# Performance work log

Measured on AMD Instinct MI355X. Metric: run time of the kernel, lower is better.

The kernel has to match this reference:

```python
import jax, jax.numpy as jnp
import numpy as np

NUM_HEADS = 8
OUT_DIM = 32


def setup_inputs() -> dict:
    key = jax.random.key(0)
    ks = jax.random.split(key, 9)
    N, E, IN = 50000, 800000, 256
    HD = NUM_HEADS * OUT_DIM
    s = 1.0 / np.sqrt(IN)
    return {
        "h": jax.random.normal(ks[0], (N, IN), jnp.float32),
        "Wq": jax.random.normal(ks[1], (HD, IN), jnp.float32) * s,
        "bq": jax.random.normal(ks[2], (HD,), jnp.float32) * 0.01,
        "Wk": jax.random.normal(ks[3], (HD, IN), jnp.float32) * s,
        "bk": jax.random.normal(ks[4], (HD,), jnp.float32) * 0.01,
        "Wv": jax.random.normal(ks[5], (HD, IN), jnp.float32) * s,
        "bv": jax.random.normal(ks[6], (HD,), jnp.float32) * 0.01,
        "src": jax.random.randint(ks[7], (E,), 0, N, jnp.int32),
        "dst": jax.random.randint(ks[8], (E,), 0, N, jnp.int32),
    }


def reference(h, Wq, bq, Wk, bk, Wv, bv, src, dst):
    N = h.shape[0]
    H, D = NUM_HEADS, OUT_DIM
    # node projections -> [N, H, D]
    Q = (h @ Wq.T + bq).reshape(N, H, D)
    K = (h @ Wk.T + bk).reshape(N, H, D)
    V = (h @ Wv.T + bv).reshape(N, H, D)
    scale = jnp.asarray(np.sqrt(D), h.dtype)
    # per-edge scores: dot(K[src], Q[dst]) over D -> [E, H]
    score = jnp.exp(jnp.clip((K[src] * Q[dst]).sum(-1) / scale, -5.0, 5.0))
    # segment-softmax denominator over destination nodes -> [N, H]
    z = jax.ops.segment_sum(score, dst, num_segments=N)
    alpha = score / z[dst]  # [E, H]; every edge's dst has z > 0
    # weighted aggregation: sum over in-edges of alpha * V[src] -> [N, H, D]
    wV = jax.ops.segment_sum(V[src] * alpha[:, :, None], dst, num_segments=N)
    return wV
```

## Files before the change

### kernel.cpp

```cpp
#include <hip/hip_runtime.h>
#include <hip/hip_bf16.h>


typedef __attribute__((ext_vector_type(8))) short short8;
typedef __attribute__((ext_vector_type(8))) unsigned short ushortx8;
typedef __attribute__((ext_vector_type(4))) unsigned short ushortx4;
typedef __attribute__((ext_vector_type(4))) float floatx4;
typedef __attribute__((ext_vector_type(4))) int intx4;

__device__ __forceinline__ void g2l16(const void* g, void* l) {
    __builtin_amdgcn_global_load_lds(
        (const __attribute__((address_space(1))) unsigned int*)g,
        (__attribute__((address_space(3))) unsigned int*)l, 16, 0, 0);
}

__device__ __forceinline__ float bf2f(unsigned short u) {
    union { unsigned int i; float f; } c; c.i = ((unsigned int)u) << 16; return c.f;
}
__device__ __forceinline__ unsigned short f2bf(float f) {
    __hip_bfloat16 b = __float2bfloat16(f);
    return *reinterpret_cast<unsigned short*>(&b);
}

__global__ __launch_bounds__(256) void cvt_bf16(const float* __restrict__ src,
                                                unsigned short* __restrict__ dst, int n4) {
    int i = blockIdx.x * 256 + threadIdx.x;
    if (i >= n4) return;
    floatx4 f = __builtin_nontemporal_load((const floatx4*)src + i);
    ushortx4 u;
    u.x = f2bf(f.x); u.y = f2bf(f.y); u.z = f2bf(f.z); u.w = f2bf(f.w);
    ((ushortx4*)dst)[i] = u;
}

__global__ __launch_bounds__(256) void cvt_w3(const float* __restrict__ Wq,
                                              const float* __restrict__ Wk,
                                              const float* __restrict__ Wv,
                                              unsigned short* __restrict__ Wb, int n4) {
    int mat = blockIdx.y;
    const float* src = (mat == 0) ? Wq : (mat == 1) ? Wk : Wv;
    int i = blockIdx.x * 256 + threadIdx.x;
    if (i >= n4) return;
    floatx4 f = __builtin_nontemporal_load((const floatx4*)src + i);
    ushortx4 u;
    u.x = f2bf(f.x); u.y = f2bf(f.y); u.z = f2bf(f.z); u.w = f2bf(f.w);
    ((ushortx4*)(Wb + (size_t)mat * 65536))[i] = u;
}

__global__ __launch_bounds__(256) void qkv_gemm_mfma(
    const unsigned short* __restrict__ hb, const unsigned short* __restrict__ Wb,
    const float* __restrict__ bq, const float* __restrict__ bk, const float* __restrict__ bv,
    unsigned short* __restrict__ Qb, unsigned short* __restrict__ KV, int N)
{
    __shared__ unsigned short Ast[2][128 * 32];
    __shared__ unsigned short Bst[2][128 * 32];

    const int tid = threadIdx.x;
    const int wave = tid >> 6;
    const int lane = tid & 63;
    const int m = lane & 15;
    const int q = lane >> 4;
    const int wr = wave >> 1, wc = wave & 1;

    const int mbase = blockIdx.x * 128;
    const int mat = blockIdx.y >> 1;
    const int colbase = (blockIdx.y & 1) * 128;
    const int wrow0 = blockIdx.y * 128;

    const float* bias = (mat == 0) ? bq : (mat == 1) ? bk : bv;

    floatx4 acc[4][4] = {};

    for (int kk = 0; kk < 256; kk += 64) {
#pragma unroll
        for (int c = 0; c < 2; c++) {
#pragma unroll
            for (int t = 0; t < 2; t++) {
                int f = t * 256 + tid;
                int row = f >> 2, kc = f & 3;
                int grow = mbase + row; if (grow > N - 1) grow = N - 1;
                g2l16(hb + (size_t)grow * 256 + kk + c * 32 + kc * 8,
                      Ast[c] + (size_t)(t * 256 + wave * 64) * 8);
            }
#pragma unroll
            for (int t = 0; t < 2; t++) {
                int f = t * 256 + tid;
                int row = f >> 2, kc = f & 3;
                g2l16(Wb + (size_t)(wrow0 + row) * 256 + kk + c * 32 + kc * 8,
                      Bst[c] + (size_t)(t * 256 + wave * 64) * 8);
            }
        }
        __syncthreads();

#pragma unroll
        for (int c = 0; c < 2; c++) {
            short8 a[4], b[4];
#pragma unroll
            for (int i = 0; i < 4; i++) {
                int r = wr * 64 + i * 16 + m;
                a[i] = *(const short8*)&Ast[c][r * 32 + q * 8];
            }
#pragma unroll
            for (int j = 0; j < 4; j++) {
                int cc = wc * 64 + j * 16 + m;
                b[j] = *(const short8*)&Bst[c][cc * 32 + q * 8];
            }
#pragma unroll
            for (int i = 0; i < 4; i++)
#pragma unroll
                for (int j = 0; j < 4; j++)
                    acc[i][j] = __builtin_amdgcn_mfma_f32_16x16x32_bf16(a[i], b[j], acc[i][j], 0, 0, 0);
        }
        __syncthreads();
    }

    float bvj[4];
#pragma unroll
    for (int j = 0; j < 4; j++) bvj[j] = bias[colbase + wc * 64 + j * 16 + m];

    const int col0 = colbase + wc * 64 + m;
#pragma unroll
    for (int i = 0; i < 4; i++) {
#pragma unroll
        for (int r = 0; r < 4; r++) {
            int grow = mbase + wr * 64 + i * 16 + q * 4 + r;
            if (grow < N) {
                if (mat == 0) {
                    unsigned short* op = Qb + (size_t)grow * 256 + col0;
#pragma unroll
                    for (int j = 0; j < 4; j++)
                        __builtin_nontemporal_store(f2bf(acc[i][j][r] + bvj[j]), op + j * 16);
                } else {
                    unsigned short* op = KV + (size_t)grow * 512 + ((mat == 2) ? 256 : 0) + col0;
#pragma unroll
                    for (int j = 0; j < 4; j++)
                        op[j * 16] = f2bf(acc[i][j][r] + bvj[j]);
                }
            }
        }
    }
}

__global__ void count_deg(const int* __restrict__ dst, int* __restrict__ deg, int E) {
    int e4 = (blockIdx.x * 256 + threadIdx.x) * 4;
    if (e4 + 3 < E) {
        intx4 d = __builtin_nontemporal_load((const intx4*)(dst + e4));
        atomicAdd(&deg[d.x], 1); atomicAdd(&deg[d.y], 1);
        atomicAdd(&deg[d.z], 1); atomicAdd(&deg[d.w], 1);
    } else {
        for (int e = e4; e < E; e++) atomicAdd(&deg[dst[e]], 1);
    }
}

#define SCAN_CHUNK 2048

__global__ void scan_phase1(const int* __restrict__ deg, int* __restrict__ partials, int N) {
    __shared__ int sdata[256];
    int base = blockIdx.x * SCAN_CHUNK;
    int sum = 0;
#pragma unroll
    for (int i = 0; i < 8; i++) {
        int idx = base + threadIdx.x + i * 256;
        if (idx < N) sum += deg[idx];
    }
    sdata[threadIdx.x] = sum;
    __syncthreads();
    for (int s = 128; s > 0; s >>= 1) {
        if (threadIdx.x < (unsigned)s) sdata[threadIdx.x] += sdata[threadIdx.x + s];
        __syncthreads();
    }
    if (threadIdx.x == 0) partials[blockIdx.x] = sdata[0];
}

__global__ void scan_phase2(int* __restrict__ partials, int nb) {
    if (threadIdx.x == 0 && blockIdx.x == 0) {
        int run = 0;
        for (int i = 0; i < nb; i++) { int v = partials[i]; partials[i] = run; run += v; }
    }
}

__global__ void scan_phase3(const int* __restrict__ deg, const int* __restrict__ partials,
                            int* __restrict__ offsets, int* __restrict__ cursor, int N, int E) {
    __shared__ int sdata[256];
    int base = blockIdx.x * SCAN_CHUNK;
    int vals[8];
    int sum = 0;
#pragma unroll
    for (int i = 0; i < 8; i++) {
        int idx = base + threadIdx.x * 8 + i;
        vals[i] = (idx < N) ? deg[idx] : 0;
        sum += vals[i];
    }
    sdata[threadIdx.x] = sum;
    __syncthreads();
    for (int s = 1; s < 256; s <<= 1) {
        int v = sdata[threadIdx.x];
        int add = (threadIdx.x >= (unsigned)s) ? sdata[threadIdx.x - s] : 0;
        __syncthreads();
        sdata[threadIdx.x] = v + add;
        __syncthreads();
    }
    int excl = (threadIdx.x == 0) ? 0 : sdata[threadIdx.x - 1];
    int run = partials[blockIdx.x] + excl;
#pragma unroll
    for (int i = 0; i < 8; i++) {
        int idx = base + threadIdx.x * 8 + i;
        if (idx < N) { offsets[idx] = run; cursor[idx] = run; }
        run += vals[i];
    }
    if (blockIdx.x == 0 && threadIdx.x == 0) offsets[N] = E;
}

__global__ void scatter_edges(const int* __restrict__ dst, const int* __restrict__ src,
                              int* __restrict__ cursor, unsigned short* __restrict__ ssorted,
                              int E) {
    int e4 = (blockIdx.x * 256 + threadIdx.x) * 4;
    if (e4 + 3 < E) {
        intx4 d = __builtin_nontemporal_load((const intx4*)(dst + e4));
        intx4 s = __builtin_nontemporal_load((const intx4*)(src + e4));
        ssorted[atomicAdd(&cursor[d.x], 1)] = (unsigned short)s.x;
        ssorted[atomicAdd(&cursor[d.y], 1)] = (unsigned short)s.y;
        ssorted[atomicAdd(&cursor[d.z], 1)] = (unsigned short)s.z;
        ssorted[atomicAdd(&cursor[d.w], 1)] = (unsigned short)s.w;
    } else {
        for (int e = e4; e < E; e++)
            ssorted[atomicAdd(&cursor[dst[e]], 1)] = (unsigned short)src[e];
    }
}

__global__ __launch_bounds__(256) void edge_agg(
    const unsigned short* __restrict__ Qb, const unsigned short* __restrict__ KV,
    const int* __restrict__ offsets, const unsigned short* __restrict__ ssorted,
    float* __restrict__ out, int N)
{
    const int wave = threadIdx.x >> 6;
    const int lane = threadIdx.x & 63;
    const int half = lane >> 5;
    const int hl = lane & 31;
    const int n = blockIdx.x * 4 + wave;
    if (n >= N) return;

    float q[8];
    {
        ushortx8 qu = __builtin_nontemporal_load((const ushortx8*)(Qb + (size_t)n * 256 + hl * 8));
#pragma unroll
        for (int j = 0; j < 8; j++) q[j] = bf2f(qu[j]);
    }

    float acc[8] = {};
    float z = 0.f;
    const int beg = offsets[n], end = offsets[n + 1];
    const int len = end - beg;
    const int mid = beg + ((len + 1) >> 1);
    const float scale = 0.17677669529663687f;

    int i = half ? mid : beg;
    const int i1 = half ? end : mid;

    for (; i + 1 < i1; i += 2) {
        int s0 = __builtin_nontemporal_load(ssorted + i);
        int s1 = __builtin_nontemporal_load(ssorted + i + 1);
        const unsigned short* p0 = KV + (size_t)s0 * 512 + hl * 8;
        const unsigned short* p1 = KV + (size_t)s1 * 512 + hl * 8;
        ushortx8 k0 = *(const ushortx8*)p0;        ushortx8 v0 = *(const ushortx8*)(p0 + 256);
        ushortx8 k1 = *(const ushortx8*)p1;        ushortx8 v1 = *(const ushortx8*)(p1 + 256);

        float d0 = 0.f, d1 = 0.f;
#pragma unroll
        for (int j = 0; j < 8; j++) {
            d0 = fmaf(bf2f(k0[j]), q[j], d0);
            d1 = fmaf(bf2f(k1[j]), q[j], d1);
        }
        d0 += __shfl_xor(d0, 1); d0 += __shfl_xor(d0, 2);
        d1 += __shfl_xor(d1, 1); d1 += __shfl_xor(d1, 2);
        float e0 = __expf(fminf(5.f, fmaxf(-5.f, d0 * scale)));
        float e1 = __expf(fminf(5.f, fmaxf(-5.f, d1 * scale)));
        z += e0 + e1;
#pragma unroll
        for (int j = 0; j < 8; j++) {
            acc[j] = fmaf(e0, bf2f(v0[j]), acc[j]);
            acc[j] = fmaf(e1, bf2f(v1[j]), acc[j]);
        }
    }
    for (; i < i1; i++) {
        int s = __builtin_nontemporal_load(ssorted + i);
        const unsigned short* p = KV + (size_t)s * 512 + hl * 8;
        ushortx8 k8 = *(const ushortx8*)p;
        ushortx8 v8 = *(const ushortx8*)(p + 256);
        float d = 0.f;
#pragma unroll
        for (int j = 0; j < 8; j++) d = fmaf(bf2f(k8[j]), q[j], d);
        d += __shfl_xor(d, 1); d += __shfl_xor(d, 2);
        float sc = __expf(fminf(5.f, fmaxf(-5.f, d * scale)));
        z += sc;
#pragma unroll
        for (int j = 0; j < 8; j++) acc[j] = fmaf(sc, bf2f(v8[j]), acc[j]);
    }

    z += __shfl_xor(z, 32);
#pragma unroll
    for (int j = 0; j < 8; j++) acc[j] += __shfl_xor(acc[j], 32);

    if (half == 0) {
        float inv = (z > 0.f) ? 1.f / z : 0.f;
        floatx4 o0, o1;
        o0[0] = acc[0] * inv; o0[1] = acc[1] * inv; o0[2] = acc[2] * inv; o0[3] = acc[3] * inv;
        o1[0] = acc[4] * inv; o1[1] = acc[5] * inv; o1[2] = acc[6] * inv; o1[3] = acc[7] * inv;
        floatx4* op = (floatx4*)(out + (size_t)n * 256 + hl * 8);
        __builtin_nontemporal_store(o0, op);
        __builtin_nontemporal_store(o1, op + 1);
    }
}

extern "C" void kernel_launch(void* const* d_in, const int* in_sizes, int n_in,
                              void* d_out, int out_size, void* d_ws, size_t ws_size,
                              hipStream_t stream) {
    const float* h  = (const float*)d_in[0];
    const float* Wq = (const float*)d_in[1];
    const float* bq = (const float*)d_in[2];
    const float* Wk = (const float*)d_in[3];
    const float* bk = (const float*)d_in[4];
    const float* Wv = (const float*)d_in[5];
    const float* bv = (const float*)d_in[6];
    const int*   src = (const int*)d_in[7];
    const int*   dst = (const int*)d_in[8];
    float* out = (float*)d_out;

    const int N = in_sizes[0] / 256;
    const int E = in_sizes[7];

    size_t off = 0;
    auto alloc = [&](size_t bytes) {
        void* p = (char*)d_ws + off;
        off += (bytes + 255) & ~(size_t)255;
        return p;
    };
    unsigned short* Qb = (unsigned short*)alloc((size_t)N * 256 * 2);
    unsigned short* KV = (unsigned short*)alloc((size_t)N * 512 * 2);
    unsigned short* hb = (unsigned short*)alloc((size_t)N * 256 * 2);
    unsigned short* Wb = (unsigned short*)alloc((size_t)768 * 256 * 2);
    int* deg      = (int*)alloc((size_t)N * 4);
    int* offsets  = (int*)alloc((size_t)(N + 1) * 4);
    int* cursor   = (int*)alloc((size_t)N * 4);
    int* partials = (int*)alloc(1024 * 4);
    unsigned short* ssorted = (unsigned short*)alloc((size_t)E * 2);

    int n4h = (N * 256) / 4;
    cvt_bf16<<<(n4h + 255) / 256, 256, 0, stream>>>(h, hb, n4h);
    int n4w = (256 * 256) / 4;
    dim3 wgrid((n4w + 255) / 256, 3);
    cvt_w3<<<wgrid, 256, 0, stream>>>(Wq, Wk, Wv, Wb, n4w);

    dim3 ggrid((N + 127) / 128, 6);
    qkv_gemm_mfma<<<ggrid, 256, 0, stream>>>(hb, Wb, bq, bk, bv, Qb, KV, N);

    hipMemsetAsync(deg, 0, (size_t)N * 4, stream);
    int eblocks4 = (E + 1023) / 1024;
    count_deg<<<eblocks4, 256, 0, stream>>>(dst, deg, E);

    int nscan = (N + SCAN_CHUNK - 1) / SCAN_CHUNK;
    scan_phase1<<<nscan, 256, 0, stream>>>(deg, partials, N);
    scan_phase2<<<1, 64, 0, stream>>>(partials, nscan);
    scan_phase3<<<nscan, 256, 0, stream>>>(deg, partials, offsets, cursor, N, E);

    scatter_edges<<<eblocks4, 256, 0, stream>>>(dst, src, cursor, ssorted, E);

    int ablocks = (N + 3) / 4;
    edge_agg<<<ablocks, 256, 0, stream>>>(Qb, KV, offsets, ssorted, out, N);
}
```

Measured before the change: 366.7 us.

## Fuse h/W bf16 conversion and degree counting into one prep kernel, XCD-remap GEMM

Merges the h conversion, weight conversion and degree-count kernels into a single grid-stride prep kernel with role-partitioned blocks. This saves launches and lets the atomic degree counting overlap with the bandwidth-bound conversion. The QKV GEMM moves to a 1D grid with an XCD-aware block remapping, so consecutive tiles that share h rows land on the same XCD for L2 reuse. The cost is fewer, longer-running blocks and more complex index math.

```diff
diff --git a/kernel.cpp b/kernel.cpp
--- a/kernel.cpp
+++ b/kernel.cpp
@@ -22,28 +22,88 @@
     return *reinterpret_cast<unsigned short*>(&b);
 }
 
-__global__ __launch_bounds__(256) void cvt_bf16(const float* __restrict__ src,
-                                                unsigned short* __restrict__ dst, int n4) {
-    int i = blockIdx.x * 256 + threadIdx.x;
-    if (i >= n4) return;
-    floatx4 f = __builtin_nontemporal_load((const floatx4*)src + i);
+__device__ __forceinline__ ushortx4 cvt4(floatx4 f) {
     ushortx4 u;
     u.x = f2bf(f.x); u.y = f2bf(f.y); u.z = f2bf(f.z); u.w = f2bf(f.w);
-    ((ushortx4*)dst)[i] = u;
-}
-
-__global__ __launch_bounds__(256) void cvt_w3(const float* __restrict__ Wq,
-                                              const float* __restrict__ Wk,
-                                              const float* __restrict__ Wv,
-                                              unsigned short* __restrict__ Wb, int n4) {
-    int mat = blockIdx.y;
-    const float* src = (mat == 0) ? Wq : (mat == 1) ? Wk : Wv;
-    int i = blockIdx.x * 256 + threadIdx.x;
-    if (i >= n4) return;
-    floatx4 f = __builtin_nontemporal_load((const floatx4*)src + i);
-    ushortx4 u;
-    u.x = f2bf(f.x); u.y = f2bf(f.y); u.z = f2bf(f.z); u.w = f2bf(f.w);
-    ((ushortx4*)(Wb + (size_t)mat * 65536))[i] = u;
+    return u;
+}
+
+#define PREP_BH 1563
+#define PREP_BW 16
+#define PREP_BD 256
+
+__global__ __launch_bounds__(256) void prep(
+    const float* __restrict__ h, unsigned short* __restrict__ hb,
+    const float* __restrict__ Wq, const float* __restrict__ Wk, const float* __restrict__ Wv,
+    unsigned short* __restrict__ Wb,
+    const int* __restrict__ dst, int* __restrict__ deg,
+    int n4h, int n4w, int E)
+{
+    const int bid = blockIdx.x;
+    const int tid = threadIdx.x;
+    if (bid < PREP_BH) {
+        const int stride = PREP_BH * 256;
+        const floatx4* hs = (const floatx4*)h;
+        ushortx4* hd = (ushortx4*)hb;
+        int i = bid * 256 + tid;
+        for (; i + 3 * stride < n4h; i += 4 * stride) {
+            floatx4 f0 = __builtin_nontemporal_load(hs + i);
+            floatx4 f1 = __builtin_nontemporal_load(hs + i + stride);
+            floatx4 f2 = __builtin_nontemporal_load(hs + i + 2 * stride);
+            floatx4 f3 = __builtin_nontemporal_load(hs + i + 3 * stride);
+            hd[i] = cvt4(f0);
+            hd[i + stride] = cvt4(f1);
+            hd[i + 2 * stride] = cvt4(f2);
+            hd[i + 3 * stride] = cvt4(f3);
+        }
+        for (; i < n4h; i += stride) {
+            floatx4 f = __builtin_nontemporal_load(hs + i);
+            hd[i] = cvt4(f);
+        }
+    } else if (bid < PREP_BH + 3 * PREP_BW) {
+        int b2 = bid - PREP_BH;
+        int mat = b2 / PREP_BW;
+        const floatx4* ws = (const floatx4*)((mat == 0) ? Wq : (mat == 1) ? Wk : Wv);
+        ushortx4* wd = (ushortx4*)(Wb + (size_t)mat * 65536);
+        const int stride = PREP_BW * 256;
+        int i = (b2 % PREP_BW) * 256 + tid;
+        for (; i + 3 * stride < n4w; i += 4 * stride) {
+            floatx4 f0 = __builtin_nontemporal_load(ws + i);
+            floatx4 f1 = __builtin_nontemporal_load(ws + i + stride);
+            floatx4 f2 = __builtin_nontemporal_load(ws + i + 2 * stride);
+            floatx4 f3 = __builtin_nontemporal_load(ws + i + 3 * stride);
+            wd[i] = cvt4(f0);
+            wd[i + stride] = cvt4(f1);
+            wd[i + 2 * stride] = cvt4(f2);
+            wd[i + 3 * stride] = cvt4(f3);
+        }
+        for (; i < n4w; i += stride) {
+            floatx4 f = __builtin_nontemporal_load(ws + i);
+            wd[i] = cvt4(f);
+        }
+    } else {
+        int b3 = bid - PREP_BH - 3 * PREP_BW;
+        const int stride = PREP_BD * 256;
+        const int ne4 = E >> 2;
+        const intx4* ds = (const intx4*)dst;
+        int i = b3 * 256 + tid;
+        for (; i + stride < ne4; i += 2 * stride) {
+            intx4 d0 = __builtin_nontemporal_load(ds + i);
+            intx4 d1 = __builtin_nontemporal_load(ds + i + stride);
+            atomicAdd(&deg[d0.x], 1); atomicAdd(&deg[d0.y], 1);
+            atomicAdd(&deg[d0.z], 1); atomicAdd(&deg[d0.w], 1);
+            atomicAdd(&deg[d1.x], 1); atomicAdd(&deg[d1.y], 1);
+            atomicAdd(&deg[d1.z], 1); atomicAdd(&deg[d1.w], 1);
+        }
+        for (; i < ne4; i += stride) {
+            intx4 d = __builtin_nontemporal_load(ds + i);
+            atomicAdd(&deg[d.x], 1); atomicAdd(&deg[d.y], 1);
+            atomicAdd(&deg[d.z], 1); atomicAdd(&deg[d.w], 1);
+        }
+        if (b3 == 0 && tid == 0) {
+            for (int e = ne4 * 4; e < E; e++) atomicAdd(&deg[dst[e]], 1);
+        }
+    }
 }
 
 __global__ __launch_bounds__(256) void qkv_gemm_mfma(
@@ -61,10 +121,19 @@
     const int q = lane >> 4;
     const int wr = wave >> 1, wc = wave & 1;
 
-    const int mbase = blockIdx.x * 128;
-    const int mat = blockIdx.y >> 1;
-    const int colbase = (blockIdx.y & 1) * 128;
-    const int wrow0 = blockIdx.y * 128;
+    const int nwg = gridDim.x;
+    const int orig = blockIdx.x;
+    const int q8 = nwg >> 3, r8 = nwg & 7;
+    const int xcd = orig & 7;
+    const int wgid = (xcd < r8 ? xcd * (q8 + 1) : r8 * (q8 + 1) + (xcd - r8) * q8)
+                     + (orig >> 3);
+    const int bx = wgid / 6;
+    const int by = wgid % 6;
+
+    const int mbase = bx * 128;
+    const int mat = by >> 1;
+    const int colbase = (by & 1) * 128;
+    const int wrow0 = by * 128;
 
     const float* bias = (mat == 0) ? bq : (mat == 1) ? bk : bv;
 
@@ -137,17 +206,6 @@
                 }
             }
         }
-    }
-}
-
-__global__ void count_deg(const int* __restrict__ dst, int* __restrict__ deg, int E) {
-    int e4 = (blockIdx.x * 256 + threadIdx.x) * 4;
-    if (e4 + 3 < E) {
-        intx4 d = __builtin_nontemporal_load((const intx4*)(dst + e4));
-        atomicAdd(&deg[d.x], 1); atomicAdd(&deg[d.y], 1);
-        atomicAdd(&deg[d.z], 1); atomicAdd(&deg[d.w], 1);
-    } else {
-        for (int e = e4; e < E; e++) atomicAdd(&deg[dst[e]], 1);
     }
 }
 
@@ -344,25 +402,21 @@
     int* partials = (int*)alloc(1024 * 4);
     unsigned short* ssorted = (unsigned short*)alloc((size_t)E * 2);
 
+    hipMemsetAsync(deg, 0, (size_t)N * 4, stream);
     int n4h = (N * 256) / 4;
-    cvt_bf16<<<(n4h + 255) / 256, 256, 0, stream>>>(h, hb, n4h);
     int n4w = (256 * 256) / 4;
-    dim3 wgrid((n4w + 255) / 256, 3);
-    cvt_w3<<<wgrid, 256, 0, stream>>>(Wq, Wk, Wv, Wb, n4w);
-
-    dim3 ggrid((N + 127) / 128, 6);
-    qkv_gemm_mfma<<<ggrid, 256, 0, stream>>>(hb, Wb, bq, bk, bv, Qb, KV, N);
-
-    hipMemsetAsync(deg, 0, (size_t)N * 4, stream);
-    int eblocks4 = (E + 1023) / 1024;
-    count_deg<<<eblocks4, 256, 0, stream>>>(dst, deg, E);
+    prep<<<PREP_BH + 3 * PREP_BW + PREP_BD, 256, 0, stream>>>(
+        h, hb, Wq, Wk, Wv, Wb, dst, deg, n4h, n4w, E);
+
+    int nb6 = ((N + 127) / 128) * 6;
+    qkv_gemm_mfma<<<nb6, 256, 0, stream>>>(hb, Wb, bq, bk, bv, Qb, KV, N);
 
     int nscan = (N + SCAN_CHUNK - 1) / SCAN_CHUNK;
     scan_phase1<<<nscan, 256, 0, stream>>>(deg, partials, N);
     scan_phase2<<<1, 64, 0, stream>>>(partials, nscan);
     scan_phase3<<<nscan, 256, 0, stream>>>(deg, partials, offsets, cursor, N, E);
-
-    scatter_edges<<<eblocks4, 256, 0, stream>>>(dst, src, cursor, ssorted, E);
+    int bc = (E + 1023) / 1024;
+    scatter_edges<<<bc, 256, 0, stream>>>(dst, src, cursor, ssorted, E);
 
     int ablocks = (N + 3) / 4;
     edge_agg<<<ablocks, 256, 0, stream>>>(Qb, KV, offsets, ssorted, out, N);
```

Result: faster. 351.6 us (-4.1%).

## Fuse preprocessing, GEMM and CSR build into one cooperative persistent kernel

Applied to the files above, without the earlier changes.

Replaces the separate conversion, QKV GEMM, memset, degree count, three scan kernels and edge scatter with a single cooperative-launch persistent kernel that uses grid.sync between phases. The degree histogram now runs concurrently with the GEMM tiles on disjoint block subsets, and the scan's serial phase-2 is replaced by a per-block warp reduction of the partials. The aim is to remove many kernel launch gaps and overlap independent work. In exchange the GEMM runs on fewer persistent blocks with a grid-stride tile loop, and every phase pays grid-wide barriers.

```diff
diff --git a/kernel.cpp b/kernel.cpp
--- a/kernel.cpp
+++ b/kernel.cpp
@@ -1,5 +1,8 @@
 #include <hip/hip_runtime.h>
 #include <hip/hip_bf16.h>
+#include <hip/hip_cooperative_groups.h>
+
+namespace cg = cooperative_groups;
 
 
 typedef __attribute__((ext_vector_type(8))) short short8;
@@ -22,51 +25,42 @@
     return *reinterpret_cast<unsigned short*>(&b);
 }
 
-__global__ __launch_bounds__(256) void cvt_bf16(const float* __restrict__ src,
-                                                unsigned short* __restrict__ dst, int n4) {
-    int i = blockIdx.x * 256 + threadIdx.x;
-    if (i >= n4) return;
-    floatx4 f = __builtin_nontemporal_load((const floatx4*)src + i);
+__device__ __forceinline__ ushortx4 cvt4(floatx4 f) {
     ushortx4 u;
     u.x = f2bf(f.x); u.y = f2bf(f.y); u.z = f2bf(f.z); u.w = f2bf(f.w);
-    ((ushortx4*)dst)[i] = u;
-}
-
-__global__ __launch_bounds__(256) void cvt_w3(const float* __restrict__ Wq,
-                                              const float* __restrict__ Wk,
-                                              const float* __restrict__ Wv,
-                                              unsigned short* __restrict__ Wb, int n4) {
-    int mat = blockIdx.y;
-    const float* src = (mat == 0) ? Wq : (mat == 1) ? Wk : Wv;
-    int i = blockIdx.x * 256 + threadIdx.x;
-    if (i >= n4) return;
-    floatx4 f = __builtin_nontemporal_load((const floatx4*)src + i);
-    ushortx4 u;
-    u.x = f2bf(f.x); u.y = f2bf(f.y); u.z = f2bf(f.z); u.w = f2bf(f.w);
-    ((ushortx4*)(Wb + (size_t)mat * 65536))[i] = u;
-}
-
-__global__ __launch_bounds__(256) void qkv_gemm_mfma(
-    const unsigned short* __restrict__ hb, const unsigned short* __restrict__ Wb,
-    const float* __restrict__ bq, const float* __restrict__ bk, const float* __restrict__ bv,
-    unsigned short* __restrict__ Qb, unsigned short* __restrict__ KV, int N)
+    return u;
+}
+
+#define SCAN_CHUNK 2048
+
+struct BuildArgs {
+    const float* h; unsigned short* hb;
+    const float* Wq; const float* Wk; const float* Wv; unsigned short* Wb;
+    const int* dst; const int* src;
+    int* deg; int* partials; int* offsets; int* cursor;
+    unsigned short* ssorted;
+    const float* bq; const float* bk; const float* bv;
+    unsigned short* Qb; unsigned short* KV;
+    int N; int E; int nb6; int n4h; int G;
+};
+
+__device__ __forceinline__ void gemm_tile(
+    const BuildArgs& a, int wgid, unsigned short (*AB)[4096], int tid)
 {
-    __shared__ unsigned short Ast[2][128 * 32];
-    __shared__ unsigned short Bst[2][128 * 32];
-
-    const int tid = threadIdx.x;
     const int wave = tid >> 6;
     const int lane = tid & 63;
     const int m = lane & 15;
     const int q = lane >> 4;
     const int wr = wave >> 1, wc = wave & 1;
-
-    const int mbase = blockIdx.x * 128;
-    const int mat = blockIdx.y >> 1;
-    const int colbase = (blockIdx.y & 1) * 128;
-    const int wrow0 = blockIdx.y * 128;
-
-    const float* bias = (mat == 0) ? bq : (mat == 1) ? bk : bv;
+    const int N = a.N;
+
+    const int bx = wgid / 6;
+    const int by = wgid % 6;
+    const int mbase = bx * 128;
+    const int mat = by >> 1;
+    const int colbase = (by & 1) * 128;
+    const int wrow0 = by * 128;
+    const float* bias = (mat == 0) ? a.bq : (mat == 1) ? a.bk : a.bv;
 
     floatx4 acc[4][4] = {};
 
@@ -78,37 +72,37 @@
                 int f = t * 256 + tid;
                 int row = f >> 2, kc = f & 3;
                 int grow = mbase + row; if (grow > N - 1) grow = N - 1;
-                g2l16(hb + (size_t)grow * 256 + kk + c * 32 + kc * 8,
-                      Ast[c] + (size_t)(t * 256 + wave * 64) * 8);
+                g2l16(a.hb + (size_t)grow * 256 + kk + c * 32 + kc * 8,
+                      AB[c] + (size_t)(t * 256 + wave * 64) * 8);
             }
 #pragma unroll
             for (int t = 0; t < 2; t++) {
                 int f = t * 256 + tid;
                 int row = f >> 2, kc = f & 3;
-                g2l16(Wb + (size_t)(wrow0 + row) * 256 + kk + c * 32 + kc * 8,
-                      Bst[c] + (size_t)(t * 256 + wave * 64) * 8);
+                g2l16(a.Wb + (size_t)(wrow0 + row) * 256 + kk + c * 32 + kc * 8,
+                      AB[2 + c] + (size_t)(t * 256 + wave * 64) * 8);
             }
         }
         __syncthreads();
 
 #pragma unroll
         for (int c = 0; c < 2; c++) {
-            short8 a[4], b[4];
+            short8 av[4], bv2[4];
 #pragma unroll
             for (int i = 0; i < 4; i++) {
                 int r = wr * 64 + i * 16 + m;
-                a[i] = *(const short8*)&Ast[c][r * 32 + q * 8];
+                av[i] = *(const short8*)&AB[c][r * 32 + q * 8];
             }
 #pragma unroll
             for (int j = 0; j < 4; j++) {
                 int cc = wc * 64 + j * 16 + m;
-                b[j] = *(const short8*)&Bst[c][cc * 32 + q * 8];
+                bv2[j] = *(const short8*)&AB[2 + c][cc * 32 + q * 8];
             }
 #pragma unroll
             for (int i = 0; i < 4; i++)
 #pragma unroll
                 for (int j = 0; j < 4; j++)
-                    acc[i][j] = __builtin_amdgcn_mfma_f32_16x16x32_bf16(a[i], b[j], acc[i][j], 0, 0, 0);
+                    acc[i][j] = __builtin_amdgcn_mfma_f32_16x16x32_bf16(av[i], bv2[j], acc[i][j], 0, 0, 0);
         }
         __syncthreads();
     }
@@ -125,12 +119,12 @@
             int grow = mbase + wr * 64 + i * 16 + q * 4 + r;
             if (grow < N) {
                 if (mat == 0) {
-                    unsigned short* op = Qb + (size_t)grow * 256 + col0;
+                    unsigned short* op = a.Qb + (size_t)grow * 256 + col0;
 #pragma unroll
                     for (int j = 0; j < 4; j++)
                         __builtin_nontemporal_store(f2bf(acc[i][j][r] + bvj[j]), op + j * 16);
                 } else {
-                    unsigned short* op = KV + (size_t)grow * 512 + ((mat == 2) ? 256 : 0) + col0;
+                    unsigned short* op = a.KV + (size_t)grow * 512 + ((mat == 2) ? 256 : 0) + col0;
 #pragma unroll
                     for (int j = 0; j < 4; j++)
                         op[j * 16] = f2bf(acc[i][j][r] + bvj[j]);
@@ -140,90 +134,136 @@
     }
 }
 
-__global__ void count_deg(const int* __restrict__ dst, int* __restrict__ deg, int E) {
-    int e4 = (blockIdx.x * 256 + threadIdx.x) * 4;
-    if (e4 + 3 < E) {
-        intx4 d = __builtin_nontemporal_load((const intx4*)(dst + e4));
-        atomicAdd(&deg[d.x], 1); atomicAdd(&deg[d.y], 1);
-        atomicAdd(&deg[d.z], 1); atomicAdd(&deg[d.w], 1);
+__global__ __launch_bounds__(256, 2) void build(BuildArgs a) {
+    __shared__ unsigned short AB[4][4096];
+    cg::grid_group grid = cg::this_grid();
+    const int bid = blockIdx.x;
+    const int tid = threadIdx.x;
+    const int G = a.G;
+
+    if (bid < 32) {
+        for (int i = bid * 256 + tid; i < a.N; i += 32 * 256) a.deg[i] = 0;
+    } else if (bid < 64) {
+        const int n4w3 = 3 * 16384;
+        for (int i = (bid - 32) * 256 + tid; i < n4w3; i += 32 * 256) {
+            int mat = i >> 14, j = i & 16383;
+            const floatx4* ws = (const floatx4*)((mat == 0) ? a.Wq : (mat == 1) ? a.Wk : a.Wv);
+            ((ushortx4*)a.Wb)[i] = cvt4(__builtin_nontemporal_load(ws + j));
+        }
     } else {
-        for (int e = e4; e < E; e++) atomicAdd(&deg[dst[e]], 1);
-    }
-}
-
-#define SCAN_CHUNK 2048
-
-__global__ void scan_phase1(const int* __restrict__ deg, int* __restrict__ partials, int N) {
-    __shared__ int sdata[256];
-    int base = blockIdx.x * SCAN_CHUNK;
-    int sum = 0;
-#pragma unroll
-    for (int i = 0; i < 8; i++) {
-        int idx = base + threadIdx.x + i * 256;
-        if (idx < N) sum += deg[idx];
-    }
-    sdata[threadIdx.x] = sum;
-    __syncthreads();
-    for (int s = 128; s > 0; s >>= 1) {
-        if (threadIdx.x < (unsigned)s) sdata[threadIdx.x] += sdata[threadIdx.x + s];
+        const int stride = (G - 64) * 256;
+        const floatx4* hs = (const floatx4*)a.h;
+        ushortx4* hd = (ushortx4*)a.hb;
+        int i = (bid - 64) * 256 + tid;
+        for (; i + 3 * stride < a.n4h; i += 4 * stride) {
+            floatx4 f0 = __builtin_nontemporal_load(hs + i);
+            floatx4 f1 = __builtin_nontemporal_load(hs + i + stride);
+            floatx4 f2 = __builtin_nontemporal_load(hs + i + 2 * stride);
+            floatx4 f3 = __builtin_nontemporal_load(hs + i + 3 * stride);
+            hd[i] = cvt4(f0);
+            hd[i + stride] = cvt4(f1);
+            hd[i + 2 * stride] = cvt4(f2);
+            hd[i + 3 * stride] = cvt4(f3);
+        }
+        for (; i < a.n4h; i += stride)
+            hd[i] = cvt4(__builtin_nontemporal_load(hs + i));
+    }
+    grid.sync();
+
+    const int histB = G >> 2;
+    if (bid < histB) {
+        const int nt = histB * 256;
+        const int ne4 = a.E >> 2;
+        const intx4* ds = (const intx4*)a.dst;
+        for (int i = bid * 256 + tid; i < ne4; i += nt) {
+            intx4 d = __builtin_nontemporal_load(ds + i);
+            atomicAdd(&a.deg[d.x], 1); atomicAdd(&a.deg[d.y], 1);
+            atomicAdd(&a.deg[d.z], 1); atomicAdd(&a.deg[d.w], 1);
+        }
+        if (bid == 0 && tid == 0)
+            for (int e = ne4 * 4; e < a.E; e++) atomicAdd(&a.deg[a.dst[e]], 1);
+    } else {
+        const int ng = G - histB;
+        for (int t = bid - histB; t < a.nb6; t += ng)
+            gemm_tile(a, t, AB, tid);
+    }
+    grid.sync();
+
+    const int nscan = (a.N + SCAN_CHUNK - 1) / SCAN_CHUNK;
+    int* sdata = (int*)&AB[0][0];
+    int* sbasep = sdata + 256;
+    if (bid < nscan) {
+        int base = bid * SCAN_CHUNK;
+        int sum = 0;
+#pragma unroll
+        for (int i = 0; i < 8; i++) {
+            int idx = base + tid + i * 256;
+            if (idx < a.N) sum += a.deg[idx];
+        }
+        sdata[tid] = sum;
         __syncthreads();
-    }
-    if (threadIdx.x == 0) partials[blockIdx.x] = sdata[0];
-}
-
-__global__ void scan_phase2(int* __restrict__ partials, int nb) {
-    if (threadIdx.x == 0 && blockIdx.x == 0) {
-        int run = 0;
-        for (int i = 0; i < nb; i++) { int v = partials[i]; partials[i] = run; run += v; }
-    }
-}
-
-__global__ void scan_phase3(const int* __restrict__ deg, const int* __restrict__ partials,
-                            int* __restrict__ offsets, int* __restrict__ cursor, int N, int E) {
-    __shared__ int sdata[256];
-    int base = blockIdx.x * SCAN_CHUNK;
-    int vals[8];
-    int sum = 0;
-#pragma unroll
-    for (int i = 0; i < 8; i++) {
-        int idx = base + threadIdx.x * 8 + i;
-        vals[i] = (idx < N) ? deg[idx] : 0;
-        sum += vals[i];
-    }
-    sdata[threadIdx.x] = sum;
-    __syncthreads();
-    for (int s = 1; s < 256; s <<= 1) {
-        int v = sdata[threadIdx.x];
-        int add = (threadIdx.x >= (unsigned)s) ? sdata[threadIdx.x - s] : 0;
+        for (int s = 128; s > 0; s >>= 1) {
+            if (tid < (unsigned)s) sdata[tid] += sdata[tid + s];
+            __syncthreads();
+        }
+        if (tid == 0) a.partials[bid] = sdata[0];
+    }
+    grid.sync();
+
+    if (bid < nscan) {
+        if (tid < 64) {
+            int v = ((int)tid < nscan && (int)tid < bid) ? a.partials[tid] : 0;
+#pragma unroll
+            for (int s = 1; s < 64; s <<= 1) v += __shfl_xor(v, s);
+            if (tid == 0) sbasep[0] = v;
+        }
+        int base = bid * SCAN_CHUNK;
+        int vals[8];
+        int sum = 0;
+#pragma unroll
+        for (int i = 0; i < 8; i++) {
+            int idx = base + tid * 8 + i;
+            vals[i] = (idx < a.N) ? a.deg[idx] : 0;
+            sum += vals[i];
+        }
+        sdata[tid] = sum;
         __syncthreads();
-        sdata[threadIdx.x] = v + add;
-        __syncthreads();
-    }
-    int excl = (threadIdx.x == 0) ? 0 : sdata[threadIdx.x - 1];
-    int run = partials[blockIdx.x] + excl;
-#pragma unroll
-    for (int i = 0; i < 8; i++) {
-        int idx = base + threadIdx.x * 8 + i;
-        if (idx < N) { offsets[idx] = run; cursor[idx] = run; }
-        run += vals[i];
-    }
-    if (blockIdx.x == 0 && threadIdx.x == 0) offsets[N] = E;
-}
-
-__global__ void scatter_edges(const int* __restrict__ dst, const int* __restrict__ src,
-                              int* __restrict__ cursor, unsigned short* __restrict__ ssorted,
-                              int E) {
-    int e4 = (blockIdx.x * 256 + threadIdx.x) * 4;
-    if (e4 + 3 < E) {
-        intx4 d = __builtin_nontemporal_load((const intx4*)(dst + e4));
-        intx4 s = __builtin_nontemporal_load((const intx4*)(src + e4));
-        ssorted[atomicAdd(&cursor[d.x], 1)] = (unsigned short)s.x;
-        ssorted[atomicAdd(&cursor[d.y], 1)] = (unsigned short)s.y;
-        ssorted[atomicAdd(&cursor[d.z], 1)] = (unsigned short)s.z;
-        ssorted[atomicAdd(&cursor[d.w], 1)] = (unsigned short)s.w;
-    } else {
-        for (int e = e4; e < E; e++)
-            ssorted[atomicAdd(&cursor[dst[e]], 1)] = (unsigned short)src[e];
+        for (int s = 1; s < 256; s <<= 1) {
+            int v = sdata[tid];
+            int add = (tid >= (unsigned)s) ? sdata[tid - s] : 0;
+            __syncthreads();
+            sdata[tid] = v + add;
+            __syncthreads();
+        }
+        int excl = (tid == 0) ? 0 : sdata[tid - 1];
+        int run = sbasep[0] + excl;
+#pragma unroll
+        for (int i = 0; i < 8; i++) {
+            int idx = base + tid * 8 + i;
+            if (idx < a.N) { a.offsets[idx] = run; a.cursor[idx] = run; }
+            run += vals[i];
+        }
+    }
+    if (bid == 0 && tid == 0) a.offsets[a.N] = a.E;
+    grid.sync();
+
+    {
+        const int t = bid * 256 + tid;
+        const int nt = G * 256;
+        const int ne4 = a.E >> 2;
+        const intx4* d4 = (const intx4*)a.dst;
+        const intx4* s4 = (const intx4*)a.src;
+        for (int i = t; i < ne4; i += nt) {
+            intx4 d = __builtin_nontemporal_load(d4 + i);
+            intx4 s = __builtin_nontemporal_load(s4 + i);
+            a.ssorted[atomicAdd(&a.cursor[d.x], 1)] = (unsigned short)s.x;
+            a.ssorted[atomicAdd(&a.cursor[d.y], 1)] = (unsigned short)s.y;
+            a.ssorted[atomicAdd(&a.cursor[d.z], 1)] = (unsigned short)s.z;
+            a.ssorted[atomicAdd(&a.cursor[d.w], 1)] = (unsigned short)s.w;
+        }
+        if (t == 0)
+            for (int e = ne4 * 4; e < a.E; e++)
+                a.ssorted[atomicAdd(&a.cursor[a.dst[e]], 1)] = (unsigned short)a.src[e];
     }
 }
 
@@ -344,25 +384,32 @@
     int* partials = (int*)alloc(1024 * 4);
     unsigned short* ssorted = (unsigned short*)alloc((size_t)E * 2);
 
-    int n4h = (N * 256) / 4;
-    cvt_bf16<<<(n4h + 255) / 256, 256, 0, stream>>>(h, hb, n4h);
-    int n4w = (256 * 256) / 4;
-    dim3 wgrid((n4w + 255) / 256, 3);
-    cvt_w3<<<wgrid, 256, 0, stream>>>(Wq, Wk, Wv, Wb, n4w);
-
-    dim3 ggrid((N + 127) / 128, 6);
-    qkv_gemm_mfma<<<ggrid, 256, 0, stream>>>(hb, Wb, bq, bk, bv, Qb, KV, N);
-
-    hipMemsetAsync(deg, 0, (size_t)N * 4, stream);
-    int eblocks4 = (E + 1023) / 1024;
-    count_deg<<<eblocks4, 256, 0, stream>>>(dst, deg, E);
-
-    int nscan = (N + SCAN_CHUNK - 1) / SCAN_CHUNK;
-    scan_phase1<<<nscan, 256, 0, stream>>>(deg, partials, N);
-    scan_phase2<<<1, 64, 0, stream>>>(partials, nscan);
-    scan_phase3<<<nscan, 256, 0, stream>>>(deg, partials, offsets, cursor, N, E);
-
-    scatter_edges<<<eblocks4, 256, 0, stream>>>(dst, src, cursor, ssorted, E);
+    static int G = 0;
+    if (G == 0) {
+        int bpc = 0;
+        if (hipOccupancyMaxActiveBlocksPerMultiprocessor(&bpc, build, 256, 0) != hipSuccess || bpc < 1)
+            bpc = 1;
+        int ncu = 256;
+        hipDeviceProp_t prop;
+        if (hipGetDeviceProperties(&prop, 0) == hipSuccess && prop.multiProcessorCount > 0)
+            ncu = prop.multiProcessorCount;
+        G = bpc * ncu;
+        if (G > 1024) G = 1024;
+        if (G < 72) G = 72;
+    }
+
+    int nb6 = ((N + 127) / 128) * 6;
+    BuildArgs ba;
+    ba.h = h; ba.hb = hb; ba.Wq = Wq; ba.Wk = Wk; ba.Wv = Wv; ba.Wb = Wb;
+    ba.dst = dst; ba.src = src;
+    ba.deg = deg; ba.partials = partials; ba.offsets = offsets; ba.cursor = cursor;
+    ba.ssorted = ssorted;
+    ba.bq = bq; ba.bk = bk; ba.bv = bv;
+    ba.Qb = Qb; ba.KV = KV;
+    ba.N = N; ba.E = E; ba.nb6 = nb6; ba.n4h = (N * 256) / 4; ba.G = G;
+
+    void* params[] = { (void*)&ba };
+    hipLaunchCooperativeKernel(build, dim3(G), dim3(256), params, 0, stream);
 
     int ablocks = (N + 3) / 4;
     edge_agg<<<ablocks, 256, 0, stream>>>(Qb, KV, offsets, ssorted, out, N);
```

Result: slower. 498.1 us (+35.8%).
